# Kernel optimization log

Hardware: AMD Instinct MI355X
Metric: run time of the kernel (lower is better)

The kernel has to match this reference:

```python
import jax, jax.numpy as jnp
import numpy as np

B, T, C = 4, 2048, 1024
N_HEAD = 16
HEAD_DIM = C // N_HEAD


def setup_inputs() -> dict:
    key = jax.random.key(0)
    k1, k2, k3 = jax.random.split(key, 3)
    scale = 0.02
    x = jax.random.normal(k1, (B, T, C), dtype=jnp.float32)
    W_attn = jax.random.normal(k2, (C, 3 * C), dtype=jnp.float32) * scale
    b_attn = jnp.zeros((3 * C,), dtype=jnp.float32)
    W_proj = jax.random.normal(k3, (C, C), dtype=jnp.float32) * scale
    b_proj = jnp.zeros((C,), dtype=jnp.float32)
    return {"x": x, "W_attn": W_attn, "b_attn": b_attn, "W_proj": W_proj, "b_proj": b_proj}


def reference(x, W_attn, b_attn, W_proj, b_proj):
    Bx, Tx, Cx = x.shape
    qkv = x @ W_attn + b_attn                      # [B,T,3C]
    q, k, v = jnp.split(qkv, 3, axis=-1)
    def split_heads(t):
        return t.reshape(Bx, Tx, N_HEAD, HEAD_DIM).transpose(0, 2, 1, 3)  # [B,H,T,D]
    q, k, v = split_heads(q), split_heads(k), split_heads(v)
    att = jnp.einsum('bhqd,bhkd->bhqk', q, k) / jnp.sqrt(jnp.float32(HEAD_DIM))
    causal = jnp.tril(jnp.ones((Tx, Tx), dtype=bool))
    att = jnp.where(causal, att, jnp.float32(-jnp.inf))
    att = jax.nn.softmax(att, axis=-1)
    y = jnp.einsum('bhqk,bhkd->bhqd', att, v)      # [B,H,T,D]
    y = y.transpose(0, 2, 1, 3).reshape(Bx, Tx, Cx)
    return y @ W_proj + b_proj
```

## Files before the change

kernel.cpp:

```cpp
#include <hip/hip_runtime.h>
#include <hip/hip_bf16.h>
#include <math.h>

#define B_  4
#define T_  2048
#define C_  1024
#define NH  16
#define HD  64
#define M_  (B_ * T_)
#define N_QKV (3 * C_)
#define KDIM 1024
#define SCALE2 0.18033688011112042f

typedef __attribute__((ext_vector_type(8))) short short8;
typedef __attribute__((ext_vector_type(4))) short bs4;
typedef __attribute__((ext_vector_type(4))) float f32x4;
typedef __attribute__((ext_vector_type(16))) float f32x16;
typedef __attribute__((ext_vector_type(4))) unsigned u32x4;

__device__ __forceinline__ short f2bs(float f) {
  __hip_bfloat16 h = __float2bfloat16(f);
  return *reinterpret_cast<short*>(&h);
}
__device__ __forceinline__ unsigned packrn(float a, float b) {
  __hip_bfloat162 h = __float22bfloat162_rn(float2{a, b});
  unsigned u;
  __builtin_memcpy(&u, &h, 4);
  return u;
}

__device__ __forceinline__ void gload16(const void* g, void* l) {
  __builtin_amdgcn_global_load_lds(
      (const __attribute__((address_space(1))) void*)g,
      (__attribute__((address_space(3))) void*)l, 16, 0, 0);
}

__device__ __forceinline__ void wtrans_body(
    const float* __restrict__ W, short* __restrict__ Wt, int Ncols, int qcols,
    int bid2, int tid, short (*t)[33])
{
  const int nb = Ncols / 32;
  const int bn = bid2 % nb, bk = bid2 / nb;
  const int r = tid >> 3, c4 = (tid & 7) * 4;
  const float cs = (bn * 32 < qcols) ? SCALE2 : 1.f;
  f32x4 v = *reinterpret_cast<const f32x4*>(
      W + (size_t)(bk * 32 + r) * Ncols + bn * 32 + c4);
  #pragma unroll
  for (int j = 0; j < 4; ++j) t[r][c4 + j] = f2bs(v[j] * cs);
  __syncthreads();
  bs4 o;
  #pragma unroll
  for (int j = 0; j < 4; ++j) o[j] = t[c4 + j][r];
  *reinterpret_cast<bs4*>(Wt + (size_t)(bn * 32 + r) * KDIM + bk * 32 + c4) = o;
}

__global__ __launch_bounds__(256) void prep_kernel(
    const float* __restrict__ x,  short* __restrict__ xb,
    const float* __restrict__ Wa, short* __restrict__ WaT,
    const float* __restrict__ Wp, short* __restrict__ WpT)
{
  __shared__ short t[32][33];
  const int bid = blockIdx.x;
  const int tid = threadIdx.x;
  if (bid < 4096) {
    const int i = (bid * 256 + tid) * 8;
    f32x4 a = *reinterpret_cast<const f32x4*>(x + i);
    f32x4 b = *reinterpret_cast<const f32x4*>(x + i + 4);
    short8 o;
    #pragma unroll
    for (int j = 0; j < 4; ++j) { o[j] = f2bs(a[j]); o[4 + j] = f2bs(b[j]); }
    *reinterpret_cast<short8*>(xb + i) = o;
  } else if (bid < 7168) {
    wtrans_body(Wa, WaT, N_QKV, C_, bid - 4096, tid, t);
  } else {
    wtrans_body(Wp, WpT, C_, 0, bid - 7168, tid, t);
  }
}

template<bool OUT_BF16>
__global__ __launch_bounds__(256) void gemm128b_kernel(
    const short* __restrict__ A, const short* __restrict__ Bt,
    const float* __restrict__ bias, void* __restrict__ outptr, int N, int nq)
{
  __shared__ short As[128 * 64];
  __shared__ short Bs[128 * 64];

  const int tid  = threadIdx.x;
  const int lane = tid & 63;
  const int w    = tid >> 6;
  const int wr   = w >> 1, wc = w & 1;
  const int rl   = lane & 15, kg = lane >> 4;
  const int nblk = N >> 7;
  const int m0 = (blockIdx.x / nblk) << 7;
  const int n0 = (blockIdx.x % nblk) << 7;

  f32x4 acc[4][4] = {};

  const int srow = w * 8 + (lane >> 3);
  const int scol = ((lane & 7) ^ ((lane >> 3) & 7)) * 8;
  const short* pa = A  + (size_t)(m0 + srow) * KDIM + scol;
  const short* pb = Bt + (size_t)(n0 + srow) * KDIM + scol;

  for (int k0 = 0; k0 < KDIM; k0 += 64) {
    __syncthreads();
    #pragma unroll
    for (int i = 0; i < 4; ++i) {
      gload16(pa + (size_t)i * 32 * KDIM + k0, &As[i * 2048 + w * 512]);
      gload16(pb + (size_t)i * 32 * KDIM + k0, &Bs[i * 2048 + w * 512]);
    }
    __syncthreads();

    #pragma unroll
    for (int kk = 0; kk < 2; ++kk) {
      const int sl = ((kk * 4 + kg) ^ (rl & 7)) * 8;
      short8 af[4], bf[4];
      #pragma unroll
      for (int i = 0; i < 4; ++i) {
        af[i] = *reinterpret_cast<short8*>(&As[(wr * 64 + i * 16 + rl) * 64 + sl]);
        bf[i] = *reinterpret_cast<short8*>(&Bs[(wc * 64 + i * 16 + rl) * 64 + sl]);
      }
      #pragma unroll
      for (int mi = 0; mi < 4; ++mi)
        #pragma unroll
        for (int ni = 0; ni < 4; ++ni)
          acc[mi][ni] = __builtin_amdgcn_mfma_f32_16x16x32_bf16(
              af[mi], bf[ni], acc[mi][ni], 0, 0, 0);
    }
  }

  #pragma unroll
  for (int ni = 0; ni < 4; ++ni) {
    const int col = n0 + wc * 64 + ni * 16 + rl;
    float bv = bias[col];
    if (col < nq) bv *= SCALE2;
    #pragma unroll
    for (int mi = 0; mi < 4; ++mi) {
      #pragma unroll
      for (int r = 0; r < 4; ++r) {
        const int row = m0 + wr * 64 + mi * 16 + kg * 4 + r;
        const float v = acc[mi][ni][r] + bv;
        if constexpr (OUT_BF16)
          ((short*)outptr)[(size_t)row * N + col] = f2bs(v);
        else
          ((float*)outptr)[(size_t)row * N + col] = v;
      }
    }
  }
}

__global__ __launch_bounds__(256) void attn_mfma11_kernel(
    const short* __restrict__ qkv, short* __restrict__ y)
{
  __shared__ short Ks[2][64 * 64];
  __shared__ short Vt[2][64 * 64];

  const int tid  = threadIdx.x;
  const int lane = tid & 63;
  const int w    = tid >> 6;
  const int q32  = lane & 31;
  const int hi   = lane >> 5;

  const int bid  = blockIdx.x;
  const int qi   = 15 - (bid >> 6);
  const int bh   = bid & 63;
  const int b    = bh >> 4, h = bh & 15;
  const size_t bT = (size_t)b * T_;

  const int kr0 = tid >> 3;
  const int kl0 = (tid & 7) ^ ((tid >> 3) & 7);
  const int kr1 = (tid + 256) >> 3;
  const int kl1 = (tid & 7) ^ (((tid + 256) >> 3) & 7);
  const size_t kbase0 = (bT + kr0) * N_QKV + C_ + h * HD + kl0 * 8;
  const size_t kbase1 = (bT + kr1) * N_QKV + C_ + h * HD + kl1 * 8;
  short* const kdst0 = &Ks[0][(w * 64) * 8];
  short* const kdst1 = &Ks[0][(w * 64 + 256) * 8];

  const int kp = tid & 31;
  const int d0 = (tid >> 5) * 8;
  const size_t vbaseA = (bT + 2 * kp) * N_QKV + 2 * C_ + h * HD + d0;
  const size_t vbaseB = vbaseA + N_QKV;
  const int vws = ((kp >> 2) << 3) + ((kp & 3) << 1);

  const int ksl = q32 & 7;

  const int nkb = 2 * qi + 2;
  const int wq0 = qi * 128 + w * 32;
  const int q   = wq0 + q32;

  short8 qf[4];
  #pragma unroll
  for (int kd = 0; kd < 4; ++kd)
    qf[kd] = *reinterpret_cast<const short8*>(
        qkv + (bT + q) * N_QKV + h * HD + kd * 16 + hi * 8);

  f32x16 o0 = {}, o1 = {};
  float m_ = -INFINITY, l_ = 0.f;

  {
    gload16(qkv + kbase0, kdst0);
    gload16(qkv + kbase1, kdst1);
    short8 va = *reinterpret_cast<const short8*>(qkv + vbaseA);
    short8 vb = *reinterpret_cast<const short8*>(qkv + vbaseB);
    #pragma unroll
    for (int j = 0; j < 8; ++j) {
      unsigned pw = (unsigned)(unsigned short)va[j] |
                    ((unsigned)(unsigned short)vb[j] << 16);
      *reinterpret_cast<unsigned*>(
          &Vt[0][(d0 + j) * 64 + (vws ^ (j << 3))]) = pw;
    }
  }
  __syncthreads();

  int cur = 0;
  for (int kb = 0; kb < nkb; ++kb) {
    const bool more = (kb + 1 < nkb);
    short8 va, vb;
    if (more) {
      const size_t koff = (size_t)(kb + 1) * 64 * N_QKV;
      gload16(qkv + kbase0 + koff, kdst0 + (cur ^ 1) * 4096);
      gload16(qkv + kbase1 + koff, kdst1 + (cur ^ 1) * 4096);
      va = *reinterpret_cast<const short8*>(qkv + vbaseA + koff);
      vb = *reinterpret_cast<const short8*>(qkv + vbaseB + koff);
    }

    const int kmin = kb * 64;
    if (kmin <= wq0 + 31) {
      const short* ksc = &Ks[cur][0];
      const short* vtc = &Vt[cur][0];

      f32x16 s0 = {}, s1 = {};
      #pragma unroll
      for (int kd = 0; kd < 4; ++kd) {
        const int sl = ((2 * kd + hi) ^ ksl) * 8;
        short8 kf0 = *reinterpret_cast<const short8*>(&ksc[q32 * 64 + sl]);
        short8 kf1 = *reinterpret_cast<const short8*>(&ksc[(32 + q32) * 64 + sl]);
        s0 = __builtin_amdgcn_mfma_f32_32x32x16_bf16(kf0, qf[kd], s0, 0, 0, 0);
        s1 = __builtin_amdgcn_mfma_f32_32x32x16_bf16(kf1, qf[kd], s1, 0, 0, 0);
      }

      if (kmin + 63 > wq0) {
        const int qrel = q - kmin - 4 * hi;
        #pragma unroll
        for (int e = 0; e < 16; ++e) {
          const int ko = (e & 3) + 8 * (e >> 2);
          if (ko > qrel)      s0[e] = -INFINITY;
          if (ko + 32 > qrel) s1[e] = -INFINITY;
        }
      }

      float mx = s0[0];
      #pragma unroll
      for (int e = 1; e < 16; ++e) mx = fmaxf(mx, s0[e]);
      #pragma unroll
      for (int e = 0; e < 16; ++e) mx = fmaxf(mx, s1[e]);
      mx = fmaxf(mx, __shfl_xor(mx, 32, 64));

      if (!__all(mx <= m_ + 8.f)) {
        const float mn = fmaxf(m_, mx);
        const float cr = exp2f(m_ - mn);
        m_ = mn;
        l_ *= cr;
        #pragma unroll
        for (int e = 0; e < 16; ++e) { o0[e] *= cr; o1[e] *= cr; }
      }

      float rs = 0.f;
      #pragma unroll
      for (int e = 0; e < 16; ++e) {
        s0[e] = exp2f(s0[e] - m_); rs += s0[e];
        s1[e] = exp2f(s1[e] - m_); rs += s1[e];
      }
      rs += __shfl_xor(rs, 32, 64);
      l_ += rs;

      unsigned pk[2][4][2], sw[2][4][2];
      #pragma unroll
      for (int gg = 0; gg < 4; ++gg)
        #pragma unroll
        for (int p = 0; p < 2; ++p) {
          pk[0][gg][p] = packrn(s0[4 * gg + 2 * p], s0[4 * gg + 2 * p + 1]);
          pk[1][gg][p] = packrn(s1[4 * gg + 2 * p], s1[4 * gg + 2 * p + 1]);
          sw[0][gg][p] = (unsigned)__shfl_xor((int)pk[0][gg][p], 32, 64);
          sw[1][gg][p] = (unsigned)__shfl_xor((int)pk[1][gg][p], 32, 64);
        }

      #pragma unroll
      for (int kk = 0; kk < 4; ++kk) {
        const int c = kk >> 1, a2 = 2 * (kk & 1);
        u32x4 t;
        t[0] = hi ? sw[c][a2 + 1][0] : pk[c][a2][0];
        t[1] = hi ? sw[c][a2 + 1][1] : pk[c][a2][1];
        t[2] = hi ? pk[c][a2 + 1][0] : sw[c][a2][0];
        t[3] = hi ? pk[c][a2 + 1][1] : sw[c][a2][1];
        const short8 pb = __builtin_bit_cast(short8, t);
        const int sl = ((2 * kk + hi) ^ ksl) * 8;
        short8 vf0 = *reinterpret_cast<const short8*>(&vtc[q32 * 64 + sl]);
        short8 vf1 = *reinterpret_cast<const short8*>(&vtc[(32 + q32) * 64 + sl]);
        o0 = __builtin_amdgcn_mfma_f32_32x32x16_bf16(vf0, pb, o0, 0, 0, 0);
        o1 = __builtin_amdgcn_mfma_f32_32x32x16_bf16(vf1, pb, o1, 0, 0, 0);
      }
    }

    if (more) {
      #pragma unroll
      for (int j = 0; j < 8; ++j) {
        unsigned pw = (unsigned)(unsigned short)va[j] |
                      ((unsigned)(unsigned short)vb[j] << 16);
        *reinterpret_cast<unsigned*>(
            &Vt[cur ^ 1][(d0 + j) * 64 + (vws ^ (j << 3))]) = pw;
      }
    }
    __syncthreads();
    cur ^= 1;
  }

  const float inv = 1.f / l_;
  short* const yp = y + (bT + q) * C_ + h * HD;
  #pragma unroll
  for (int gg = 0; gg < 4; ++gg) {
    bs4 ov0, ov1;
    #pragma unroll
    for (int t = 0; t < 4; ++t) {
      ov0[t] = f2bs(o0[4 * gg + t] * inv);
      ov1[t] = f2bs(o1[4 * gg + t] * inv);
    }
    *reinterpret_cast<bs4*>(yp + 8 * gg + 4 * hi)      = ov0;
    *reinterpret_cast<bs4*>(yp + 32 + 8 * gg + 4 * hi) = ov1;
  }
}

extern "C" void kernel_launch(void* const* d_in, const int* in_sizes, int n_in,
                              void* d_out, int out_size, void* d_ws, size_t ws_size,
                              hipStream_t stream) {
  const float* x  = (const float*)d_in[0];
  const float* Wa = (const float*)d_in[1];
  const float* ba = (const float*)d_in[2];
  const float* Wp = (const float*)d_in[3];
  const float* bp = (const float*)d_in[4];

  short* qkvb = (short*)d_ws;
  short* xb   = qkvb + (size_t)M_ * N_QKV;
  short* yb   = xb;
  short* WaT  = xb + (size_t)M_ * C_;
  short* WpT  = WaT + (size_t)N_QKV * KDIM;

  prep_kernel<<<8192, 256, 0, stream>>>(x, xb, Wa, WaT, Wp, WpT);
  gemm128b_kernel<true><<<(M_ / 128) * (N_QKV / 128), 256, 0, stream>>>(
      xb, WaT, ba, qkvb, N_QKV, C_);
  attn_mfma11_kernel<<<16 * B_ * NH, 256, 0, stream>>>(qkvb, yb);
  gemm128b_kernel<false><<<(M_ / 128) * (C_ / 128), 256, 0, stream>>>(
      yb, WpT, bp, d_out, C_, 0);
}
```

Baseline: 197.5 us.

## Split long causal attention rows across two blocks and merge partials

For the eight longest query tiles, the key range is split into two halves processed by separate blocks. Each block writes unnormalized fp32 partial outputs plus row max and sum to workspace. A new merge kernel combines them with log-sum-exp rescaling. The aim is better load balance across CUs on the causal triangle, at the cost of extra global traffic, one more kernel launch, and a dependence on the workspace being large enough.

```diff
diff --git a/kernel.cpp b/kernel.cpp
--- a/kernel.cpp
+++ b/kernel.cpp
@@ -148,8 +148,9 @@
   }
 }
 
-__global__ __launch_bounds__(256) void attn_mfma11_kernel(
-    const short* __restrict__ qkv, short* __restrict__ y)
+__global__ __launch_bounds__(256) void attn_mfma12_kernel(
+    const short* __restrict__ qkv, short* __restrict__ y,
+    float* __restrict__ Opart, float* __restrict__ LMpart, int split)
 {
   __shared__ short Ks[2][64 * 64];
   __shared__ short Vt[2][64 * 64];
@@ -161,29 +162,48 @@
   const int hi   = lane >> 5;
 
   const int bid  = blockIdx.x;
-  const int qi   = 15 - (bid >> 6);
-  const int bh   = bid & 63;
-  const int b    = bh >> 4, h = bh & 15;
+  int qi, kb0, kb1, pbid;
+  bool part;
+  if (split) {
+    if (bid < 1024) {
+      const int s = bid >> 6;
+      qi = 15 - (s >> 1);
+      const int nk = qi + 1;
+      kb0 = (s & 1) ? nk : 0;
+      kb1 = (s & 1) ? 2 * nk : nk;
+      part = true; pbid = bid;
+    } else {
+      qi = 7 - ((bid - 1024) >> 6);
+      kb0 = 0; kb1 = 2 * qi + 2;
+      part = false; pbid = 0;
+    }
+  } else {
+    qi = 15 - (bid >> 6);
+    kb0 = 0; kb1 = 2 * qi + 2;
+    part = false; pbid = 0;
+  }
+  const int bh = bid & 63;
+  const int b  = bh >> 4, h = bh & 15;
   const size_t bT = (size_t)b * T_;
+  const size_t koff0 = (size_t)kb0 * 64 * N_QKV;
 
   const int kr0 = tid >> 3;
   const int kl0 = (tid & 7) ^ ((tid >> 3) & 7);
   const int kr1 = (tid + 256) >> 3;
   const int kl1 = (tid & 7) ^ (((tid + 256) >> 3) & 7);
-  const size_t kbase0 = (bT + kr0) * N_QKV + C_ + h * HD + kl0 * 8;
-  const size_t kbase1 = (bT + kr1) * N_QKV + C_ + h * HD + kl1 * 8;
+  const size_t kbase0 = (bT + kr0) * N_QKV + C_ + h * HD + kl0 * 8 + koff0;
+  const size_t kbase1 = (bT + kr1) * N_QKV + C_ + h * HD + kl1 * 8 + koff0;
   short* const kdst0 = &Ks[0][(w * 64) * 8];
   short* const kdst1 = &Ks[0][(w * 64 + 256) * 8];
 
   const int kp = tid & 31;
   const int d0 = (tid >> 5) * 8;
-  const size_t vbaseA = (bT + 2 * kp) * N_QKV + 2 * C_ + h * HD + d0;
+  const size_t vbaseA = (bT + 2 * kp) * N_QKV + 2 * C_ + h * HD + d0 + koff0;
   const size_t vbaseB = vbaseA + N_QKV;
   const int vws = ((kp >> 2) << 3) + ((kp & 3) << 1);
 
   const int ksl = q32 & 7;
 
-  const int nkb = 2 * qi + 2;
   const int wq0 = qi * 128 + w * 32;
   const int q   = wq0 + q32;
 
@@ -212,11 +232,11 @@
   __syncthreads();
 
   int cur = 0;
-  for (int kb = 0; kb < nkb; ++kb) {
-    const bool more = (kb + 1 < nkb);
+  for (int kb = kb0; kb < kb1; ++kb) {
+    const bool more = (kb + 1 < kb1);
     short8 va, vb;
     if (more) {
-      const size_t koff = (size_t)(kb + 1) * 64 * N_QKV;
+      const size_t koff = (size_t)(kb + 1 - kb0) * 64 * N_QKV;
       gload16(qkv + kbase0 + koff, kdst0 + (cur ^ 1) * 4096);
       gload16(qkv + kbase1 + koff, kdst1 + (cur ^ 1) * 4096);
       va = *reinterpret_cast<const short8*>(qkv + vbaseA + koff);
@@ -314,18 +334,73 @@
     cur ^= 1;
   }
 
-  const float inv = 1.f / l_;
-  short* const yp = y + (bT + q) * C_ + h * HD;
+  if (!part) {
+    const float inv = 1.f / l_;
+    short* const yp = y + (bT + q) * C_ + h * HD;
+    #pragma unroll
+    for (int gg = 0; gg < 4; ++gg) {
+      bs4 ov0, ov1;
+      #pragma unroll
+      for (int t = 0; t < 4; ++t) {
+        ov0[t] = f2bs(o0[4 * gg + t] * inv);
+        ov1[t] = f2bs(o1[4 * gg + t] * inv);
+      }
+      *reinterpret_cast<bs4*>(yp + 8 * gg + 4 * hi)      = ov0;
+      *reinterpret_cast<bs4*>(yp + 32 + 8 * gg + 4 * hi) = ov1;
+    }
+  } else {
+    float* const op = Opart + (size_t)pbid * 8192 + (size_t)(w * 32 + q32) * 64;
+    #pragma unroll
+    for (int gg = 0; gg < 4; ++gg) {
+      f32x4 a, c;
+      #pragma unroll
+      for (int t = 0; t < 4; ++t) { a[t] = o0[4 * gg + t]; c[t] = o1[4 * gg + t]; }
+      *reinterpret_cast<f32x4*>(op + 8 * gg + 4 * hi)      = a;
+      *reinterpret_cast<f32x4*>(op + 32 + 8 * gg + 4 * hi) = c;
+    }
+    if (hi == 0) {
+      LMpart[pbid * 256 + (w * 32 + q32)]       = l_;
+      LMpart[pbid * 256 + 128 + (w * 32 + q32)] = m_;
+    }
+  }
+}
+
+__global__ __launch_bounds__(256) void attn_merge_kernel(
+    const float* __restrict__ Opart, const float* __restrict__ LMpart,
+    short* __restrict__ y)
+{
+  const int mb = blockIdx.x;
+  const int s2 = mb >> 6, bh = mb & 63;
+  const int qi = 15 - s2;
+  const int bidA = (2 * s2) * 64 + bh;
+  const int bidB = (2 * s2 + 1) * 64 + bh;
+  const int t  = threadIdx.x;
+  const int r  = t >> 1;
+  const int dh = (t & 1) * 32;
+
+  const float lA = LMpart[bidA * 256 + r];
+  const float mA = LMpart[bidA * 256 + 128 + r];
+  const float lB = LMpart[bidB * 256 + r];
+  const float mB = LMpart[bidB * 256 + 128 + r];
+  const float m  = fmaxf(mA, mB);
+  const float eA = exp2f(mA - m);
+  const float eB = exp2f(mB - m);
+  const float inv = 1.f / (lA * eA + lB * eB);
+
+  const float* oA = Opart + (size_t)bidA * 8192 + r * 64 + dh;
+  const float* oB = Opart + (size_t)bidB * 8192 + r * 64 + dh;
+  const int b = bh >> 4, h = bh & 15;
+  short* yp = y + ((size_t)b * T_ + qi * 128 + r) * C_ + h * HD + dh;
+
   #pragma unroll
-  for (int gg = 0; gg < 4; ++gg) {
-    bs4 ov0, ov1;
-    #pragma unroll
-    for (int t = 0; t < 4; ++t) {
-      ov0[t] = f2bs(o0[4 * gg + t] * inv);
-      ov1[t] = f2bs(o1[4 * gg + t] * inv);
-    }
-    *reinterpret_cast<bs4*>(yp + 8 * gg + 4 * hi)      = ov0;
-    *reinterpret_cast<bs4*>(yp + 32 + 8 * gg + 4 * hi) = ov1;
+  for (int j = 0; j < 8; ++j) {
+    f32x4 va = *reinterpret_cast<const f32x4*>(oA + 4 * j);
+    f32x4 vb = *reinterpret_cast<const f32x4*>(oB + 4 * j);
+    bs4 o;
+    #pragma unroll
+    for (int t2 = 0; t2 < 4; ++t2)
+      o[t2] = f2bs((va[t2] * eA + vb[t2] * eB) * inv);
+    *reinterpret_cast<bs4*>(yp + 4 * j) = o;
   }
 }
 
@@ -343,11 +418,17 @@
   short* yb   = xb;
   short* WaT  = xb + (size_t)M_ * C_;
   short* WpT  = WaT + (size_t)N_QKV * KDIM;
+  float* Opart  = (float*)((char*)d_ws + 75497472);
+  float* LMpart = Opart + (size_t)1024 * 8192;
+  const int split = (ws_size >= 110100480u) ? 1 : 0;
 
   prep_kernel<<<8192, 256, 0, stream>>>(x, xb, Wa, WaT, Wp, WpT);
   gemm128b_kernel<true><<<(M_ / 128) * (N_QKV / 128), 256, 0, stream>>>(
       xb, WaT, ba, qkvb, N_QKV, C_);
-  attn_mfma11_kernel<<<16 * B_ * NH, 256, 0, stream>>>(qkvb, yb);
+  attn_mfma12_kernel<<<split ? 1536 : 1024, 256, 0, stream>>>(
+      qkvb, yb, Opart, LMpart, split);
+  if (split)
+    attn_merge_kernel<<<512, 256, 0, stream>>>(Opart, LMpart, yb);
   gemm128b_kernel<false><<<(M_ / 128) * (C_ / 128), 256, 0, stream>>>(
       yb, WpT, bp, d_out, C_, 0);
 }
```

Result: slower. 215.5 us (+9.1%).
